# Optimization experiments

Measured on AMD Instinct MI355X. Metric: run time of the kernel, lower is better.

The kernel has to match this reference:

```python
import jax, jax.numpy as jnp
import numpy as np

B, S, E = 4, 4096, 1024
HEADS, WINDOW = 16, 128
HEAD_DIM = E // HEADS


def setup_inputs() -> dict:
    key = jax.random.key(0)
    ks = jax.random.split(key, 6)
    x = jax.random.normal(ks[0], (B, S, E), dtype=jnp.float32)
    attn_mask = jnp.ones((B, 1, S), dtype=jnp.float32)
    scale = 1.0 / np.sqrt(E)
    Wq = jax.random.normal(ks[1], (E, E), dtype=jnp.float32) * scale
    Wk = jax.random.normal(ks[2], (E, E), dtype=jnp.float32) * scale
    Wv = jax.random.normal(ks[3], (E, E), dtype=jnp.float32) * scale
    Wo = jax.random.normal(ks[4], (E, E), dtype=jnp.float32) * scale
    return {"x": x, "attn_mask": attn_mask, "Wq": Wq, "Wk": Wk, "Wv": Wv, "Wo": Wo}


def _look_around(t, axis_windows=2):
    # t: [..., nw, w, ...]; returns concat of windows [i-1, i, i+1] along the
    # intra-window axis, zero-padded at the boundaries.
    pad = [(0, 0)] * t.ndim
    pad[axis_windows] = (1, 1)
    tp = jnp.pad(t, pad)
    nw = t.shape[axis_windows]
    def sl(start):
        idx = [slice(None)] * t.ndim
        idx[axis_windows] = slice(start, start + nw)
        return tp[tuple(idx)]
    return jnp.concatenate([sl(0), sl(1), sl(2)], axis=axis_windows + 1)


def _local_attention(q, k, v, key_mask, window):
    # q,k,v: [b, h, n, d]; key_mask: [b, n] bool. Non-causal, look_backward=1,
    # look_forward=1 (lucidrains LocalAttention defaults for causal=False).
    b, h, n, d = q.shape
    nw = n // window
    scale = d ** -0.5
    qb = q.reshape(b, h, nw, window, d) * scale
    kb = k.reshape(b, h, nw, window, d)
    vb = v.reshape(b, h, nw, window, d)
    k_look = _look_around(kb, axis_windows=2)  # [b,h,nw,3w,d]
    v_look = _look_around(vb, axis_windows=2)
    # mask: user key mask AND in-bounds (padded boundary windows are invalid)
    mb = key_mask.reshape(b, nw, window)
    m_look = _look_around(mb, axis_windows=1)  # [b,nw,3w]
    m_look = m_look[:, None, :, None, :]       # [b,1,nw,1,3w]
    scores = jnp.einsum('bhnwd,bhnkd->bhnwk', qb, k_look)
    mask_value = -jnp.finfo(scores.dtype).max
    scores = jnp.where(m_look, scores, mask_value)
    attn = jax.nn.softmax(scores, axis=-1)
    out = jnp.einsum('bhnwk,bhnkd->bhnwd', attn, v_look)
    return out.reshape(b, h, n, d)


def reference(x, attn_mask, Wq, Wk, Wv, Wo):
    b, c, e = x.shape
    h, d = HEADS, HEAD_DIM
    q = jnp.einsum('bce,ef->bcf', x, Wq.T).reshape(b, c, h, d).transpose(0, 2, 1, 3)
    k = jnp.einsum('bce,ef->bcf', x, Wk.T).reshape(b, c, h, d).transpose(0, 2, 1, 3)
    v = jnp.einsum('bce,ef->bcf', x, Wv.T).reshape(b, c, h, d).transpose(0, 2, 1, 3)
    key_mask = attn_mask[:, 0, :] > 0  # [b, c] bool
    attended = _local_attention(q, k, v, key_mask, WINDOW)
    attended = attended.transpose(0, 2, 1, 3).reshape(b, c, h * d)
    return jnp.einsum('bcf,fe->bce', attended, Wo.T)
```

## Files before the change

### kernel.cpp

```cpp
#include <hip/hip_runtime.h>
#include <stdint.h>

typedef __bf16 bf16_t;
typedef __bf16 bf16x8 __attribute__((ext_vector_type(8)));
typedef __bf16 bf16x4 __attribute__((ext_vector_type(4)));
typedef float f32x4 __attribute__((ext_vector_type(4)));

__device__ __forceinline__ f32x4 mfma16(bf16x8 a, bf16x8 b, f32x4 c) {
  return __builtin_amdgcn_mfma_f32_16x16x32_bf16(a, b, c, 0, 0, 0);
}

__device__ __forceinline__ void g2l16(const void* g, void* l) {
  __builtin_amdgcn_global_load_lds((const __attribute__((address_space(1))) void*)g,
                                   (__attribute__((address_space(3))) void*)l, 16, 0, 0);
}

#define FENCE() asm volatile("" ::: "memory")

__global__ void __launch_bounds__(256) cvt_f32_bf16(const float* __restrict__ in,
                                                    bf16_t* __restrict__ out) {
  long i = ((long)blockIdx.x * 256 + threadIdx.x) * 8;
  float4 f0 = *(const float4*)(in + i);
  float4 f1 = *(const float4*)(in + i + 4);
  bf16x8 v;
  v[0] = (bf16_t)f0.x; v[1] = (bf16_t)f0.y; v[2] = (bf16_t)f0.z; v[3] = (bf16_t)f0.w;
  v[4] = (bf16_t)f1.x; v[5] = (bf16_t)f1.y; v[6] = (bf16_t)f1.z; v[7] = (bf16_t)f1.w;
  *(bf16x8*)(out + i) = v;
}

__global__ void __launch_bounds__(256) cvt_weights(const float* __restrict__ Wq,
                                                   const float* __restrict__ Wk,
                                                   const float* __restrict__ Wv,
                                                   const float* __restrict__ Wo,
                                                   bf16_t* __restrict__ wqk,
                                                   bf16_t* __restrict__ wvb,
                                                   bf16_t* __restrict__ wob) {
  const int id = blockIdx.x;
  const int seg = id >> 9, off = id & 511;
  const float* src;
  bf16_t* dst;
  if (seg == 0)      { src = Wq; dst = wqk; }
  else if (seg == 1) { src = Wk; dst = wqk + 1048576; }
  else if (seg == 2) { src = Wv; dst = wvb; }
  else               { src = Wo; dst = wob; }
  long i = ((long)off * 256 + threadIdx.x) * 8;
  float4 f0 = *(const float4*)(src + i);
  float4 f1 = *(const float4*)(src + i + 4);
  bf16x8 v;
  v[0] = (bf16_t)f0.x; v[1] = (bf16_t)f0.y; v[2] = (bf16_t)f0.z; v[3] = (bf16_t)f0.w;
  v[4] = (bf16_t)f1.x; v[5] = (bf16_t)f1.y; v[6] = (bf16_t)f1.z; v[7] = (bf16_t)f1.w;
  *(bf16x8*)(dst + i) = v;
}

template <typename OutT>
__device__ __forceinline__ void gemm_core(const bf16_t* __restrict__ A,
                                          const bf16_t* __restrict__ Bt,
                                          OutT* __restrict__ C,
                                          int N, int K, int NBN, int nseg, int flat,
                                          char* smem) {
  const int t = threadIdx.x;
  const int w = t >> 6, l = t & 63;
  const int lr = l & 15, lg = l >> 4;
  const int wm = w >> 2, wn = w & 3;

  const int swz = (flat & 7) * (nseg >> 3) + (flat >> 3);
  const int bm = swz / NBN, bn = swz % NBN;
  const long rowA0 = (long)bm * 256;
  const long colC0 = (long)bn * 256;
  const int KT = K >> 6;

  const int colSwz = ((l & 7) ^ (l >> 3)) * 8;
  const bf16_t* gA = A + (rowA0 + w * 32 + (l >> 3)) * (long)K + colSwz;
  const bf16_t* gB = Bt + (colC0 + w * 32 + (l >> 3)) * (long)K + colSwz;
  const long K8 = (long)K * 8;

  const int sx0 = (lg ^ (lr & 7)) * 16;
  const int sx1 = ((4 + lg) ^ (lr & 7)) * 16;
  const int aRow = (wm * 128 + lr) * 128;
  const int bRow = 32768 + (wn * 64 + lr) * 128;

  f32x4 acc[8][4] = {};

#define STAGE_A(buf, kt)                                          \
  {                                                               \
    char* _d = smem + (buf) * 65536 + w * 4096;                   \
    const long _ko = (long)(kt) * 64;                             \
    g2l16(gA + _ko, _d);                                          \
    g2l16(gA + K8 + _ko, _d + 1024);                              \
    g2l16(gA + 2 * K8 + _ko, _d + 2048);                          \
    g2l16(gA + 3 * K8 + _ko, _d + 3072);                          \
  }
#define STAGE_B(buf, kt)                                          \
  {                                                               \
    char* _d = smem + (buf) * 65536 + 32768 + w * 4096;           \
    const long _ko = (long)(kt) * 64;                             \
    g2l16(gB + _ko, _d);                                          \
    g2l16(gB + K8 + _ko, _d + 1024);                              \
    g2l16(gB + 2 * K8 + _ko, _d + 2048);                          \
    g2l16(gB + 3 * K8 + _ko, _d + 3072);                          \
  }

  STAGE_A(0, 0); STAGE_B(0, 0);
  FENCE();
  asm volatile("s_waitcnt vmcnt(0)" ::: "memory");
  __builtin_amdgcn_s_barrier();

  for (int kt = 0; kt < KT; ++kt) {
    const char* sb = smem + (kt & 1) * 65536;
    const int nb = (kt + 1) & 1;
    const bool ds = (kt + 1) < KT;

    bf16x8 bfr[4][2];

    {
      bf16x8 a0[4][2];
#pragma unroll
      for (int j = 0; j < 4; ++j) {
        bfr[j][0] = *(const bf16x8*)(sb + bRow + j * 2048 + sx0);
        bfr[j][1] = *(const bf16x8*)(sb + bRow + j * 2048 + sx1);
      }
#pragma unroll
      for (int i = 0; i < 4; ++i) {
        a0[i][0] = *(const bf16x8*)(sb + aRow + i * 2048 + sx0);
        a0[i][1] = *(const bf16x8*)(sb + aRow + i * 2048 + sx1);
      }
      if (ds) STAGE_A(nb, kt + 1);
      FENCE();
      __builtin_amdgcn_s_barrier();
      asm volatile("s_waitcnt lgkmcnt(0)" ::: "memory");
      __builtin_amdgcn_sched_barrier(0);
      __builtin_amdgcn_s_setprio(1);
#pragma unroll
      for (int i = 0; i < 4; ++i)
#pragma unroll
        for (int j = 0; j < 4; ++j) {
          acc[i][j] = mfma16(a0[i][0], bfr[j][0], acc[i][j]);
          acc[i][j] = mfma16(a0[i][1], bfr[j][1], acc[i][j]);
        }
      __builtin_amdgcn_s_setprio(0);
      __builtin_amdgcn_sched_barrier(0);
      FENCE();
      __builtin_amdgcn_s_barrier();
    }

    {
      bf16x8 a1[4][2];
#pragma unroll
      for (int i = 0; i < 4; ++i) {
        a1[i][0] = *(const bf16x8*)(sb + aRow + (4 + i) * 2048 + sx0);
        a1[i][1] = *(const bf16x8*)(sb + aRow + (4 + i) * 2048 + sx1);
      }
      if (ds) STAGE_B(nb, kt + 1);
      FENCE();
      __builtin_amdgcn_s_barrier();
      asm volatile("s_waitcnt lgkmcnt(0)" ::: "memory");
      __builtin_amdgcn_sched_barrier(0);
      __builtin_amdgcn_s_setprio(1);
#pragma unroll
      for (int i = 0; i < 4; ++i)
#pragma unroll
        for (int j = 0; j < 4; ++j) {
          acc[4 + i][j] = mfma16(a1[i][0], bfr[j][0], acc[4 + i][j]);
          acc[4 + i][j] = mfma16(a1[i][1], bfr[j][1], acc[4 + i][j]);
        }
      __builtin_amdgcn_s_setprio(0);
      __builtin_amdgcn_sched_barrier(0);
      FENCE();
      if (ds) {
        asm volatile("s_waitcnt vmcnt(0)" ::: "memory");
      }
      __builtin_amdgcn_s_barrier();
    }
  }
#undef STAGE_A
#undef STAGE_B

#pragma unroll
  for (int i = 0; i < 8; ++i)
#pragma unroll
    for (int j = 0; j < 4; ++j)
#pragma unroll
      for (int r = 0; r < 4; ++r) {
        long row = rowA0 + wm * 128 + i * 16 + lg * 4 + r;
        long col = colC0 + wn * 64 + j * 16 + lr;
        C[row * (long)N + col] = (OutT)acc[i][j][r];
      }
}

__global__ void __launch_bounds__(512, 2) gemm_qkvt(const bf16_t* __restrict__ xb,
                                                    const bf16_t* __restrict__ wqk,
                                                    bf16_t* __restrict__ qk,
                                                    const bf16_t* __restrict__ wvb,
                                                    bf16_t* __restrict__ vt) {
  extern __shared__ char smem[];
  const int id = blockIdx.x;
  if (id < 512) {
    gemm_core<bf16_t>(xb, wqk, qk, 2048, 1024, 8, 512, id, smem);
  } else {
    gemm_core<bf16_t>(wvb, xb, vt, 16384, 1024, 64, 256, id - 512, smem);
  }
}

__global__ void __launch_bounds__(512, 2) gemm_out(const bf16_t* __restrict__ att,
                                                   const bf16_t* __restrict__ wob,
                                                   float* __restrict__ out) {
  extern __shared__ char smem[];
  gemm_core<float>(att, wob, out, 1024, 1024, 4, 256, blockIdx.x, smem);
}

__global__ void __launch_bounds__(512, 4) swa3(const bf16_t* __restrict__ QK,
                                               const bf16_t* __restrict__ VT,
                                               const float* __restrict__ amask,
                                               bf16_t* __restrict__ Att) {
  extern __shared__ char lds[];
  bf16_t* Ks = (bf16_t*)lds;
  bf16_t* Vs = (bf16_t*)(lds + 16384);
  float* bias = (float*)(lds + 32768);
  const int t = threadIdx.x, w = t >> 6, l = t & 63, lr = l & 15, lg = l >> 4;
  char* Psw = lds + 34304 + w * 4352;

  const int idx = (blockIdx.x & 7) * 256 + (blockIdx.x >> 3);
  const int n = idx & 31, h = (idx >> 5) & 15, b = idx >> 9;
  const long rowQ = (long)b * 4096 + n * 128;

  bf16x8 qf[2];
#pragma unroll
  for (int ks = 0; ks < 2; ++ks)
    qf[ks] = *(const bf16x8*)&QK[(rowQ + w * 16 + lr) * 2048 + h * 64 + ks * 32 + lg * 8];

  f32x4 oT[4] = {};
  float l_run = 0.f;

  const int kcLo = (n > 0) ? n - 1 : 0;
  const int kcHi = (n < 31) ? n + 1 : 31;
  const long kbase0 = (long)b * 4096 + (long)kcLo * 128;
  const int nch = kcHi - kcLo + 1;

  const int kcol = ((t & 7) ^ ((t >> 3) & 7)) * 8;
  const bf16_t* gK0 = QK + (kbase0 + (t >> 3)) * 2048 + 1024 + h * 64 + kcol;
  const int vrow = t >> 4;
  const int vcol = ((t & 15) ^ ((t >> 4) & 15)) * 8;
  const bf16_t* gV0 = VT + ((long)h * 64 + vrow) * 16384 + kbase0 + vcol;

  bf16_t* lK0 = Ks + t * 8;
  bf16_t* lK1 = Ks + 4096 + t * 8;
  bf16_t* lV0 = Vs + t * 8;
  bf16_t* lV1 = Vs + 4096 + t * 8;

#define STAGE_K(cc)                                               \
  {                                                               \
    const bf16_t* _k = gK0 + (long)(cc) * 128 * 2048;             \
    g2l16(_k, lK0);                                               \
    g2l16(_k + (long)64 * 2048, lK1);                             \
  }
#define STAGE_V(cc)                                               \
  {                                                               \
    const bf16_t* _v = gV0 + (long)(cc) * 128;                    \
    g2l16(_v, lV0);                                               \
    g2l16(_v + (long)32 * 16384, lV1);                            \
  }

  STAGE_K(0); STAGE_V(0);
  if (t < nch * 32) {
    float4 mv = *(const float4*)(amask + kbase0 + t * 4);
    float4 bv;
    bv.x = mv.x > 0.f ? 0.f : -1e30f;
    bv.y = mv.y > 0.f ? 0.f : -1e30f;
    bv.z = mv.z > 0.f ? 0.f : -1e30f;
    bv.w = mv.w > 0.f ? 0.f : -1e30f;
    *(float4*)&bias[t * 4] = bv;
  }
  FENCE();
  asm volatile("s_waitcnt vmcnt(0)" ::: "memory");
  __syncthreads();

  const float c1 = 0.18033688011112042f;

  for (int c = 0; c < nch; ++c) {
    const bool more = (c + 1) < nch;

    f32x4 s[8];
#pragma unroll
    for (int kb = 0; kb < 8; ++kb) {
      f32x4 z = {};
#pragma unroll
      for (int ks = 0; ks < 2; ++ks) {
        bf16x8 kA = *(const bf16x8*)&Ks[(kb * 16 + lr) * 64 + (((ks * 4 + lg) ^ (lr & 7)) * 8)];
        z = mfma16(kA, qf[ks], z);
      }
      s[kb] = z;
    }
    FENCE();
    __builtin_amdgcn_s_barrier();
    if (more) STAGE_K(c + 1);

    float rs = 0.f;
#pragma unroll
    for (int kb = 0; kb < 8; ++kb) {
      f32x4 bb = *(const f32x4*)&bias[c * 128 + kb * 16 + lg * 4];
#pragma unroll
      for (int r = 0; r < 4; ++r) {
        float p = __builtin_amdgcn_exp2f(s[kb][r] * c1 + bb[r]);
        s[kb][r] = p;
        rs += p;
      }
    }
    rs += __shfl_xor(rs, 16);
    rs += __shfl_xor(rs, 32);
    l_run += rs;

#pragma unroll
    for (int kb = 0; kb < 8; ++kb) {
      bf16x4 pv;
      pv[0] = (bf16_t)s[kb][0]; pv[1] = (bf16_t)s[kb][1];
      pv[2] = (bf16_t)s[kb][2]; pv[3] = (bf16_t)s[kb][3];
      *(bf16x4*)(Psw + lr * 272 + kb * 32 + lg * 8) = pv;
    }
    asm volatile("s_waitcnt lgkmcnt(0)" ::: "memory");
    __builtin_amdgcn_sched_barrier(0);

    FENCE();
    if (more) asm volatile("s_waitcnt vmcnt(2)" ::: "memory");
    else      asm volatile("s_waitcnt vmcnt(0)" ::: "memory");
    __builtin_amdgcn_s_barrier();

#pragma unroll
    for (int ks = 0; ks < 4; ++ks) {
      bf16x8 pB = *(const bf16x8*)(Psw + lr * 272 + ks * 64 + lg * 16);
#pragma unroll
      for (int df = 0; df < 4; ++df) {
        bf16x8 vA = *(const bf16x8*)&Vs[(df * 16 + lr) * 128 + (((ks * 4 + lg) ^ lr) * 8)];
        oT[df] = mfma16(vA, pB, oT[df]);
      }
    }
    FENCE();
    __builtin_amdgcn_s_barrier();
    if (more) {
      STAGE_V(c + 1);
      FENCE();
      asm volatile("s_waitcnt vmcnt(2)" ::: "memory");
      __builtin_amdgcn_s_barrier();
    }
  }
#undef STAGE_K
#undef STAGE_V

  float inv = 1.f / l_run;
#pragma unroll
  for (int df = 0; df < 4; ++df) {
    bf16x4 ov;
#pragma unroll
    for (int r = 0; r < 4; ++r) ov[r] = (bf16_t)(oT[df][r] * inv);
    *(bf16x4*)(Psw + lr * 272 + df * 32 + lg * 8) = ov;
  }
  asm volatile("s_waitcnt lgkmcnt(0)" ::: "memory");
  __builtin_amdgcn_sched_barrier(0);
  const char* myP = lds + 34304 + w * 4352;
  bf16x8 r0 = *(const bf16x8*)(myP + (l >> 2) * 272 + (l & 3) * 32);
  bf16x8 r1 = *(const bf16x8*)(myP + (l >> 2) * 272 + (l & 3) * 32 + 16);
  long orow = rowQ + w * 16 + (l >> 2);
  bf16_t* op = Att + orow * 1024 + h * 64 + (l & 3) * 16;
  *(bf16x8*)op = r0;
  *(bf16x8*)(op + 8) = r1;
}

extern "C" void kernel_launch(void* const* d_in, const int* in_sizes, int n_in,
                              void* d_out, int out_size, void* d_ws, size_t ws_size,
                              hipStream_t stream) {
  const float* x  = (const float*)d_in[0];
  const float* am = (const float*)d_in[1];
  const float* Wq = (const float*)d_in[2];
  const float* Wk = (const float*)d_in[3];
  const float* Wv = (const float*)d_in[4];
  const float* Wo = (const float*)d_in[5];
  float* out = (float*)d_out;

  char* ws = (char*)d_ws;
  bf16_t* qk  = (bf16_t*)ws;
  bf16_t* vt  = (bf16_t*)(ws + 67108864);
  bf16_t* xbx = (bf16_t*)(ws + 100663296);
  bf16_t* wqk = (bf16_t*)(ws + 134217728);
  bf16_t* wvb = (bf16_t*)(ws + 138412032);
  bf16_t* wob = (bf16_t*)(ws + 140509184);

  const int kSmemG = 131072;
  hipFuncSetAttribute(reinterpret_cast<const void*>(&gemm_qkvt),
                      hipFuncAttributeMaxDynamicSharedMemorySize, kSmemG);
  hipFuncSetAttribute(reinterpret_cast<const void*>(&gemm_out),
                      hipFuncAttributeMaxDynamicSharedMemorySize, kSmemG);
  const int kSmemS = 69120;
  hipFuncSetAttribute(reinterpret_cast<const void*>(&swa3),
                      hipFuncAttributeMaxDynamicSharedMemorySize, kSmemS);

  cvt_f32_bf16<<<8192, 256, 0, stream>>>(x, xbx);
  cvt_weights<<<2048, 256, 0, stream>>>(Wq, Wk, Wv, Wo, wqk, wvb, wob);

  gemm_qkvt<<<768, 512, kSmemG, stream>>>(xbx, wqk, qk, wvb, vt);

  swa3<<<2048, 512, kSmemS, stream>>>(qk, vt, am, xbx);

  gemm_out<<<256, 512, kSmemG, stream>>>(xbx, wob, out);
}
```

Measured before the change: 212.9 us.

## Read K/V directly from global in window attention and merge convert kernels

The attention kernel no longer stages K and V chunks into LDS with async global-to-LDS copies and barriers. Each wave now loads its MFMA operands straight from global memory, relying on L2/L1 caching. This cuts the LDS footprint and removes the per-chunk barriers, which may allow more blocks per CU. The trade-off is that 8 waves re-read the same K/V data from cache without a coalesced swizzle. Separately, the input and weight fp32-to-bf16 conversions are merged into a single launch to save one kernel launch.

```diff
diff --git a/kernel.cpp b/kernel.cpp
--- a/kernel.cpp
+++ b/kernel.cpp
@@ -17,33 +17,30 @@
 
 #define FENCE() asm volatile("" ::: "memory")
 
-__global__ void __launch_bounds__(256) cvt_f32_bf16(const float* __restrict__ in,
-                                                    bf16_t* __restrict__ out) {
-  long i = ((long)blockIdx.x * 256 + threadIdx.x) * 8;
-  float4 f0 = *(const float4*)(in + i);
-  float4 f1 = *(const float4*)(in + i + 4);
-  bf16x8 v;
-  v[0] = (bf16_t)f0.x; v[1] = (bf16_t)f0.y; v[2] = (bf16_t)f0.z; v[3] = (bf16_t)f0.w;
-  v[4] = (bf16_t)f1.x; v[5] = (bf16_t)f1.y; v[6] = (bf16_t)f1.z; v[7] = (bf16_t)f1.w;
-  *(bf16x8*)(out + i) = v;
-}
-
-__global__ void __launch_bounds__(256) cvt_weights(const float* __restrict__ Wq,
-                                                   const float* __restrict__ Wk,
-                                                   const float* __restrict__ Wv,
-                                                   const float* __restrict__ Wo,
-                                                   bf16_t* __restrict__ wqk,
-                                                   bf16_t* __restrict__ wvb,
-                                                   bf16_t* __restrict__ wob) {
+__global__ void __launch_bounds__(256) cvt_all(const float* __restrict__ x,
+                                               const float* __restrict__ Wq,
+                                               const float* __restrict__ Wk,
+                                               const float* __restrict__ Wv,
+                                               const float* __restrict__ Wo,
+                                               bf16_t* __restrict__ xb,
+                                               bf16_t* __restrict__ wqk,
+                                               bf16_t* __restrict__ wvb,
+                                               bf16_t* __restrict__ wob) {
   const int id = blockIdx.x;
-  const int seg = id >> 9, off = id & 511;
   const float* src;
   bf16_t* dst;
-  if (seg == 0)      { src = Wq; dst = wqk; }
-  else if (seg == 1) { src = Wk; dst = wqk + 1048576; }
-  else if (seg == 2) { src = Wv; dst = wvb; }
-  else               { src = Wo; dst = wob; }
-  long i = ((long)off * 256 + threadIdx.x) * 8;
+  long off;
+  if (id < 8192) {
+    src = x; dst = xb; off = (long)id;
+  } else {
+    const int seg = (id - 8192) >> 9;
+    off = (id - 8192) & 511;
+    if (seg == 0)      { src = Wq; dst = wqk; }
+    else if (seg == 1) { src = Wk; dst = wqk + 1048576; }
+    else if (seg == 2) { src = Wv; dst = wvb; }
+    else               { src = Wo; dst = wob; }
+  }
+  long i = (off * 256 + threadIdx.x) * 8;
   float4 f0 = *(const float4*)(src + i);
   float4 f1 = *(const float4*)(src + i + 4);
   bf16x8 v;
@@ -208,16 +205,14 @@
   gemm_core<float>(att, wob, out, 1024, 1024, 4, 256, blockIdx.x, smem);
 }
 
-__global__ void __launch_bounds__(512, 4) swa3(const bf16_t* __restrict__ QK,
+__global__ void __launch_bounds__(512, 4) swa5(const bf16_t* __restrict__ QK,
                                                const bf16_t* __restrict__ VT,
                                                const float* __restrict__ amask,
                                                bf16_t* __restrict__ Att) {
   extern __shared__ char lds[];
-  bf16_t* Ks = (bf16_t*)lds;
-  bf16_t* Vs = (bf16_t*)(lds + 16384);
-  float* bias = (float*)(lds + 32768);
+  float* bias = (float*)lds;
   const int t = threadIdx.x, w = t >> 6, l = t & 63, lr = l & 15, lg = l >> 4;
-  char* Psw = lds + 34304 + w * 4352;
+  char* Psw = lds + 2048 + w * 4352;
 
   const int idx = (blockIdx.x & 7) * 256 + (blockIdx.x >> 3);
   const int n = idx & 31, h = (idx >> 5) & 15, b = idx >> 9;
@@ -236,31 +231,6 @@
   const long kbase0 = (long)b * 4096 + (long)kcLo * 128;
   const int nch = kcHi - kcLo + 1;
 
-  const int kcol = ((t & 7) ^ ((t >> 3) & 7)) * 8;
-  const bf16_t* gK0 = QK + (kbase0 + (t >> 3)) * 2048 + 1024 + h * 64 + kcol;
-  const int vrow = t >> 4;
-  const int vcol = ((t & 15) ^ ((t >> 4) & 15)) * 8;
-  const bf16_t* gV0 = VT + ((long)h * 64 + vrow) * 16384 + kbase0 + vcol;
-
-  bf16_t* lK0 = Ks + t * 8;
-  bf16_t* lK1 = Ks + 4096 + t * 8;
-  bf16_t* lV0 = Vs + t * 8;
-  bf16_t* lV1 = Vs + 4096 + t * 8;
-
-#define STAGE_K(cc)                                               \
-  {                                                               \
-    const bf16_t* _k = gK0 + (long)(cc) * 128 * 2048;             \
-    g2l16(_k, lK0);                                               \
-    g2l16(_k + (long)64 * 2048, lK1);                             \
-  }
-#define STAGE_V(cc)                                               \
-  {                                                               \
-    const bf16_t* _v = gV0 + (long)(cc) * 128;                    \
-    g2l16(_v, lV0);                                               \
-    g2l16(_v + (long)32 * 16384, lV1);                            \
-  }
-
-  STAGE_K(0); STAGE_V(0);
   if (t < nch * 32) {
     float4 mv = *(const float4*)(amask + kbase0 + t * 4);
     float4 bv;
@@ -270,14 +240,13 @@
     bv.w = mv.w > 0.f ? 0.f : -1e30f;
     *(float4*)&bias[t * 4] = bv;
   }
-  FENCE();
-  asm volatile("s_waitcnt vmcnt(0)" ::: "memory");
   __syncthreads();
 
   const float c1 = 0.18033688011112042f;
 
   for (int c = 0; c < nch; ++c) {
-    const bool more = (c + 1) < nch;
+    const bf16_t* Kc = QK + (kbase0 + (long)c * 128) * 2048 + 1024 + h * 64;
+    const bf16_t* Vc = VT + (long)h * 64 * 16384 + kbase0 + (long)c * 128;
 
     f32x4 s[8];
 #pragma unroll
@@ -285,14 +254,11 @@
       f32x4 z = {};
 #pragma unroll
       for (int ks = 0; ks < 2; ++ks) {
-        bf16x8 kA = *(const bf16x8*)&Ks[(kb * 16 + lr) * 64 + (((ks * 4 + lg) ^ (lr & 7)) * 8)];
+        bf16x8 kA = *(const bf16x8*)&Kc[(kb * 16 + lr) * 2048 + ks * 32 + lg * 8];
         z = mfma16(kA, qf[ks], z);
       }
       s[kb] = z;
     }
-    FENCE();
-    __builtin_amdgcn_s_barrier();
-    if (more) STAGE_K(c + 1);
 
     float rs = 0.f;
 #pragma unroll
@@ -319,32 +285,19 @@
     asm volatile("s_waitcnt lgkmcnt(0)" ::: "memory");
     __builtin_amdgcn_sched_barrier(0);
 
-    FENCE();
-    if (more) asm volatile("s_waitcnt vmcnt(2)" ::: "memory");
-    else      asm volatile("s_waitcnt vmcnt(0)" ::: "memory");
-    __builtin_amdgcn_s_barrier();
-
 #pragma unroll
     for (int ks = 0; ks < 4; ++ks) {
       bf16x8 pB = *(const bf16x8*)(Psw + lr * 272 + ks * 64 + lg * 16);
 #pragma unroll
       for (int df = 0; df < 4; ++df) {
-        bf16x8 vA = *(const bf16x8*)&Vs[(df * 16 + lr) * 128 + (((ks * 4 + lg) ^ lr) * 8)];
+        bf16x8 vA = *(const bf16x8*)&Vc[(long)(df * 16 + lr) * 16384 + ks * 32 + lg * 8];
         oT[df] = mfma16(vA, pB, oT[df]);
       }
     }
-    FENCE();
-    __builtin_amdgcn_s_barrier();
-    if (more) {
-      STAGE_V(c + 1);
-      FENCE();
-      asm volatile("s_waitcnt vmcnt(2)" ::: "memory");
-      __builtin_amdgcn_s_barrier();
-    }
-  }
-#undef STAGE_K
-#undef STAGE_V
-
+  }
+
+  asm volatile("s_waitcnt lgkmcnt(0)" ::: "memory");
+  __builtin_amdgcn_sched_barrier(0);
   float inv = 1.f / l_run;
 #pragma unroll
   for (int df = 0; df < 4; ++df) {
@@ -355,7 +308,7 @@
   }
   asm volatile("s_waitcnt lgkmcnt(0)" ::: "memory");
   __builtin_amdgcn_sched_barrier(0);
-  const char* myP = lds + 34304 + w * 4352;
+  const char* myP = lds + 2048 + w * 4352;
   bf16x8 r0 = *(const bf16x8*)(myP + (l >> 2) * 272 + (l & 3) * 32);
   bf16x8 r1 = *(const bf16x8*)(myP + (l >> 2) * 272 + (l & 3) * 32 + 16);
   long orow = rowQ + w * 16 + (l >> 2);
@@ -388,16 +341,15 @@
                       hipFuncAttributeMaxDynamicSharedMemorySize, kSmemG);
   hipFuncSetAttribute(reinterpret_cast<const void*>(&gemm_out),
                       hipFuncAttributeMaxDynamicSharedMemorySize, kSmemG);
-  const int kSmemS = 69120;
-  hipFuncSetAttribute(reinterpret_cast<const void*>(&swa3),
+  const int kSmemS = 36864;
+  hipFuncSetAttribute(reinterpret_cast<const void*>(&swa5),
                       hipFuncAttributeMaxDynamicSharedMemorySize, kSmemS);
 
-  cvt_f32_bf16<<<8192, 256, 0, stream>>>(x, xbx);
-  cvt_weights<<<2048, 256, 0, stream>>>(Wq, Wk, Wv, Wo, wqk, wvb, wob);
+  cvt_all<<<10240, 256, 0, stream>>>(x, Wq, Wk, Wv, Wo, xbx, wqk, wvb, wob);
 
   gemm_qkvt<<<768, 512, kSmemG, stream>>>(xbx, wqk, qk, wvb, vt);
 
-  swa3<<<2048, 512, kSmemS, stream>>>(qk, vt, am, xbx);
+  swa5<<<2048, 512, kSmemS, stream>>>(qk, vt, am, xbx);
 
   gemm_out<<<256, 512, kSmemG, stream>>>(xbx, wob, out);
 }
```

Result: slower. 340.3 us (+59.8%).
